# Performance work log

Hardware: AMD Instinct MI355X
Metric: run time of the kernel (lower is better)

The kernel has to match this reference:

```python
import jax, jax.numpy as jnp
import numpy as np

NUM_FEATURES = 1_000_000
EMB_DIM = 16
NUM_FIELDS = 39
CIN_SIZES = (200, 200, 200)
DNN_SIZES = (400, 400)


def setup_inputs() -> dict:
    key = jax.random.key(0)
    ks = jax.random.split(key, 16)
    B = 2048
    inp = {}
    inp["feature_ids"] = jax.random.randint(ks[0], (B, NUM_FIELDS), 0, NUM_FEATURES)
    inp["feature_vals"] = jax.random.uniform(ks[1], (B, NUM_FIELDS), dtype=jnp.float32)
    # embeddings (xavier-normal-ish scale)
    inp["emb"] = jax.random.normal(ks[2], (NUM_FEATURES, EMB_DIM), jnp.float32) * 0.02
    inp["bias_emb"] = jax.random.normal(ks[3], (NUM_FEATURES, 1), jnp.float32) * 0.02
    # CIN conv1d (kernel size 1) weights: (out, in)
    field_nums = [NUM_FIELDS]
    for i, size in enumerate(CIN_SIZES):
        cin_in = field_nums[-1] * NUM_FIELDS
        inp[f"cin_W{i}"] = jax.random.normal(ks[4 + i], (size, cin_in), jnp.float32) / np.sqrt(cin_in)
        inp[f"cin_b{i}"] = jnp.zeros((size,), jnp.float32)
        field_nums.append(size // 2 if i != len(CIN_SIZES) - 1 else size)
    # DNN linears: (out, in)
    last = NUM_FIELDS * EMB_DIM
    for i, size in enumerate(DNN_SIZES):
        inp[f"dnn_W{i}"] = jax.random.normal(ks[8 + i], (size, last), jnp.float32) / np.sqrt(last)
        inp[f"dnn_b{i}"] = jnp.zeros((size,), jnp.float32)
        last = size
    hidden_size = sum(CIN_SIZES[:-1]) // 2 + CIN_SIZES[-1]  # 400
    fc_in = hidden_size + DNN_SIZES[-1]
    inp["fc_W"] = jax.random.normal(ks[12], (1, fc_in), jnp.float32) / np.sqrt(fc_in)
    inp["fc_b"] = jnp.zeros((1,), jnp.float32)
    return inp


def _forward(feature_ids, feature_vals, emb, bias_emb,
             cin_W0, cin_b0, cin_W1, cin_b1, cin_W2, cin_b2,
             dnn_W0, dnn_b0, dnn_W1, dnn_b1, fc_W, fc_b):
    B = feature_ids.shape[0]
    inputs = emb[feature_ids] * feature_vals[:, :, None]        # [B, F, D]
    input_biases = bias_emb[feature_ids][..., 0] * feature_vals  # [B, F]

    # CIN
    Ws = (cin_W0, cin_W1, cin_W2)
    bs = (cin_b0, cin_b1, cin_b2)
    h = inputs
    finals = []
    n_layers = len(CIN_SIZES)
    for i in range(n_layers):
        size = CIN_SIZES[i]
        x = jnp.einsum('bhd,bmd->bhmd', h, inputs)              # [B, H, F, D]
        x = x.reshape(B, -1, EMB_DIM)                           # [B, H*F, D]
        x = jnp.einsum('bcd,oc->bod', x, Ws[i]) + bs[i][None, :, None]  # 1x1 conv
        x = jax.nn.relu(x)
        if i != n_layers - 1:
            h, direct = x[:, : size // 2], x[:, size // 2:]
        else:
            direct = x
        finals.append(direct)
    cin_result = jnp.sum(jnp.concatenate(finals, axis=1), axis=-1)  # [B, hidden]

    # DNN
    d = inputs.reshape(B, -1)
    d = jax.nn.relu(d @ dnn_W0.T + dnn_b0)
    d = jax.nn.relu(d @ dnn_W1.T + dnn_b1)

    out = (jnp.concatenate((cin_result, d), axis=1) @ fc_W.T + fc_b)[:, 0]
    return out + jnp.sum(input_biases, axis=1)                  # [B]


def reference(feature_ids, feature_vals, emb, bias_emb,
              cin_W0, cin_b0, cin_W1, cin_b1, cin_W2, cin_b2,
              dnn_W0, dnn_b0, dnn_W1, dnn_b1, fc_W, fc_b):
    return _forward(feature_ids, feature_vals, emb, bias_emb,
                    cin_W0, cin_b0, cin_W1, cin_b1, cin_W2, cin_b2,
                    dnn_W0, dnn_b0, dnn_W1, dnn_b1, fc_W, fc_b)
```

## Files before the change

kernel.cpp:

```cpp
#include <hip/hip_runtime.h>

#define B 2048
#define NF 39
#define D 16

typedef __bf16 bf16x8 __attribute__((ext_vector_type(8)));
typedef float f32x4 __attribute__((ext_vector_type(4)));

__device__ __forceinline__ void lds_barrier() {
  asm volatile("s_waitcnt lgkmcnt(0)" ::: "memory");
  __builtin_amdgcn_s_barrier();
}

__global__ __launch_bounds__(256) void gather_kernel(
    const int* __restrict__ fid, const float* __restrict__ fval,
    const float* __restrict__ emb, const float* __restrict__ bias_emb,
    float* __restrict__ inputs, float* __restrict__ biassum) {
  int b = blockIdx.x;
  __shared__ int ids[NF];
  __shared__ float vals[NF];
  int t = threadIdx.x;
  if (t < NF) { ids[t] = fid[b * NF + t]; vals[t] = fval[b * NF + t]; }
  __syncthreads();
  for (int i = t; i < NF * D; i += 256) {
    int f = i >> 4, d = i & 15;
    inputs[b * NF * D + i] = emb[(long)ids[f] * D + d] * vals[f];
  }
  if (t < 64) {
    float pb = (t < NF) ? bias_emb[ids[t]] * vals[t] : 0.f;
#pragma unroll
    for (int m = 32; m >= 1; m >>= 1) pb += __shfl_xor(pb, m);
    if (t == 0) biassum[b] = pb;
  }
}

__device__ __forceinline__ void prep_cin_one(const float* __restrict__ W,
                                             __bf16* __restrict__ Wg,
                                             int Hreal, int idx) {
  int l = idx & 63;
  int mt = (idx >> 6) % 13;
  int c = idx / (13 * 64);
  int o = mt * 16 + (l & 15);
  int kb = c * 32 + ((l >> 4) << 3);
  int rowlen = Hreal * 39;
  bf16x8 v;
#pragma unroll
  for (int j = 0; j < 8; ++j) {
    int k = kb + j;
    int h = k / 40;
    int m = k - h * 40;
    float val = 0.f;
    if (o < 200 && h < Hreal && m < 39) val = W[(long)o * rowlen + h * 39 + m];
    v[j] = (__bf16)val;
  }
  *reinterpret_cast<bf16x8*>(Wg + (long)idx * 8) = v;
}

__device__ __forceinline__ void prep_dnn_one(const float* __restrict__ W,
                                             __bf16* __restrict__ Wd,
                                             int IN, int idx) {
  int l = idx & 63;
  int tt = (idx >> 6) % 25;
  int c = idx / (25 * 64);
  int o = tt * 16 + (l & 15);
  int kb = c * 32 + ((l >> 4) << 3);
  bf16x8 v;
#pragma unroll
  for (int j = 0; j < 8; ++j) {
    int k = kb + j;
    v[j] = (k < IN) ? (__bf16)W[(long)o * IN + k] : (__bf16)0.f;
  }
  *reinterpret_cast<bf16x8*>(Wd + (long)idx * 8) = v;
}

#define PREP_T0 (50 * 13 * 64)
#define PREP_T12 (126 * 13 * 64)
#define PREP_T3 (20 * 25 * 64)
#define PREP_T4 (13 * 25 * 64)
#define PREP_TOTAL (PREP_T0 + 2 * PREP_T12 + PREP_T3 + PREP_T4)

__global__ void prep_all(const float* __restrict__ cW0, const float* __restrict__ cW1,
                         const float* __restrict__ cW2, const float* __restrict__ dW0,
                         const float* __restrict__ dW1, __bf16* __restrict__ Wg0,
                         __bf16* __restrict__ Wg1, __bf16* __restrict__ Wg2,
                         __bf16* __restrict__ Wd0, __bf16* __restrict__ Wd1) {
  int idx = blockIdx.x * 256 + threadIdx.x;
  if (idx < PREP_T0) { prep_cin_one(cW0, Wg0, 39, idx); return; }
  idx -= PREP_T0;
  if (idx < PREP_T12) { prep_cin_one(cW1, Wg1, 100, idx); return; }
  idx -= PREP_T12;
  if (idx < PREP_T12) { prep_cin_one(cW2, Wg2, 100, idx); return; }
  idx -= PREP_T12;
  if (idx < PREP_T3) { prep_dnn_one(dW0, Wd0, 624, idx); return; }
  idx -= PREP_T3;
  if (idx < PREP_T4) prep_dnn_one(dW1, Wd1, 400, idx);
}

__device__ __forceinline__ void form_x(const float* Hs, const float* Zs,
                                       __bf16* xbuf, int k0, int col) {
  int h = (int)((unsigned)k0 / 40u);
  int m0 = k0 - h * 40;
  float hv = Hs[h * 64 + col];
  const float4* zp = reinterpret_cast<const float4*>(Zs + col * 44 + m0);
  float4 za = zp[0], zb = zp[1];
  bf16x8 xv;
  xv[0] = (__bf16)(hv * za.x); xv[1] = (__bf16)(hv * za.y);
  xv[2] = (__bf16)(hv * za.z); xv[3] = (__bf16)(hv * za.w);
  xv[4] = (__bf16)(hv * zb.x); xv[5] = (__bf16)(hv * zb.y);
  xv[6] = (__bf16)(hv * zb.z); xv[7] = (__bf16)(hv * zb.w);
  int g = (k0 >> 3) & 7;
  *reinterpret_cast<bf16x8*>(
      reinterpret_cast<char*>(xbuf) + col * 128 + ((g * 16) ^ ((col & 7) << 4))) = xv;
}

template <int NW, int NST, int SPLIT>
__device__ __forceinline__ void cin_layer(
    float* Hs, const float* Zs, __bf16* Xs,
    const __bf16* __restrict__ Wg, const float* __restrict__ bias,
    float* __restrict__ cin_out, int col_offset, int bbase, int t) {
  constexpr int TLO = (13 * NW) >> 2;
  const int l = t & 63;
  const int q = l >> 4, dd = l & 15;

  f32x4 acc[13] = {};
  bf16x8 wf[8], wfn[8];
  const __bf16* wp = Wg + l * 8 + TLO * 512;
#pragma unroll
  for (int i = 0; i < 4; ++i)
#pragma unroll
    for (int hf = 0; hf < 2; ++hf)
      wf[i * 2 + hf] = *reinterpret_cast<const bf16x8*>(wp + hf * 6656 + i * 512);

  form_x(Hs, Zs, Xs, NW * 8, l);
  form_x(Hs, Zs, Xs, (NW + 4) * 8, l);
  lds_barrier();

  for (int s = 0; s < NST; ++s) {
    __bf16* xcur = Xs + (s & 1) * 4096;
    __bf16* xnxt = Xs + ((s + 1) & 1) * 4096;
    const bool more = (s + 1 < NST);
    if (more) {
      const __bf16* wq = wp + 13312;
#pragma unroll
      for (int i = 0; i < 4; ++i)
#pragma unroll
        for (int hf = 0; hf < 2; ++hf)
          wfn[i * 2 + hf] =
              *reinterpret_cast<const bf16x8*>(wq + hf * 6656 + i * 512);
    }
    bf16x8 bfr[4][2];
#pragma unroll
    for (int f = 0; f < 4; ++f)
#pragma unroll
      for (int hf = 0; hf < 2; ++hf) {
        int col = f * 16 + dd;
        int g = q + hf * 4;
        bfr[f][hf] = *reinterpret_cast<const bf16x8*>(
            reinterpret_cast<const char*>(xcur) + col * 128 +
            ((g * 16) ^ ((col & 7) << 4)));
      }
    if (more) {
      form_x(Hs, Zs, xnxt, (s + 1) * 64 + NW * 8, l);
      form_x(Hs, Zs, xnxt, (s + 1) * 64 + (NW + 4) * 8, l);
    }
    __builtin_amdgcn_s_setprio(1);
#pragma unroll
    for (int i = 0; i < 13; ++i) {
      const int p = 13 * NW + i;
      const int ti = (p >> 2) - TLO;
      const int f = p & 3;
      acc[i] = __builtin_amdgcn_mfma_f32_16x16x32_bf16(wf[ti * 2 + 0], bfr[f][0],
                                                       acc[i], 0, 0, 0);
      acc[i] = __builtin_amdgcn_mfma_f32_16x16x32_bf16(wf[ti * 2 + 1], bfr[f][1],
                                                       acc[i], 0, 0, 0);
    }
    __builtin_amdgcn_s_setprio(0);
    lds_barrier();
    if (more) {
#pragma unroll
      for (int i = 0; i < 8; ++i) wf[i] = wfn[i];
      wp += 13312;
    }
  }

#pragma unroll
  for (int i = 0; i < 13; ++i) {
    const int p = 13 * NW + i;
    const int tt = p >> 2, f = p & 3;
    const int b = bbase + f;
#pragma unroll
    for (int r = 0; r < 4; ++r) {
      int o = tt * 16 + q * 4 + r;
      if (o < 200) {
        float x = fmaxf(acc[i][r] + bias[o], 0.f);
        if (SPLIT && o < 100) {
          Hs[o * 64 + f * 16 + dd] = x;
        } else {
          x += __shfl_xor(x, 1);
          x += __shfl_xor(x, 2);
          x += __shfl_xor(x, 4);
          x += __shfl_xor(x, 8);
          if (dd == 0) cin_out[b * 400 + col_offset + o - (SPLIT ? 100 : 0)] = x;
        }
      }
    }
  }
  lds_barrier();
}

template <int NW>
__device__ __forceinline__ void cin_all(
    float* Hs, const float* Zs, __bf16* Xs, const __bf16* Wg0,
    const __bf16* Wg1, const __bf16* Wg2, const float* cb0, const float* cb1,
    const float* cb2, float* cinres, int bbase, int t) {
  cin_layer<NW, 25, 1>(Hs, Zs, Xs, Wg0, cb0, cinres, 0, bbase, t);
  cin_layer<NW, 63, 1>(Hs, Zs, Xs, Wg1, cb1, cinres, 100, bbase, t);
  cin_layer<NW, 63, 0>(Hs, Zs, Xs, Wg2, cb2, cinres, 200, bbase, t);
}

__global__ __launch_bounds__(256, 2) void cin_fused(
    const float* __restrict__ Zin, const __bf16* __restrict__ Wg0,
    const __bf16* __restrict__ Wg1, const __bf16* __restrict__ Wg2,
    const float* __restrict__ cb0, const float* __restrict__ cb1,
    const float* __restrict__ cb2, float* __restrict__ cinres) {
  __shared__ float Hs[101 * 64];
  __shared__ float Zs[64 * 44];
  __shared__ __bf16 Xs[2 * 64 * 64];
  const int t = threadIdx.x;
  const int bbase = blockIdx.x * 4;

  for (int i = t; i < 64 * 40; i += 256) {
    int col = i / 40, m = i - (i / 40) * 40;
    int b = bbase + (col >> 4), d = col & 15;
    Zs[col * 44 + m] = (m < NF) ? Zin[((long)b * NF + m) * 16 + d] : 0.f;
  }
  for (int i = t; i < 41 * 64; i += 256) {
    int h = i >> 6, col = i & 63;
    int b = bbase + (col >> 4), d = col & 15;
    Hs[i] = (h < NF) ? Zin[((long)b * NF + h) * 16 + d] : 0.f;
  }
  if (t < 64) Hs[100 * 64 + t] = 0.f;
  __syncthreads();

  const int w = t >> 6;
  if (w == 0) cin_all<0>(Hs, Zs, Xs, Wg0, Wg1, Wg2, cb0, cb1, cb2, cinres, bbase, t);
  else if (w == 1) cin_all<1>(Hs, Zs, Xs, Wg0, Wg1, Wg2, cb0, cb1, cb2, cinres, bbase, t);
  else if (w == 2) cin_all<2>(Hs, Zs, Xs, Wg0, Wg1, Wg2, cb0, cb1, cb2, cinres, bbase, t);
  else cin_all<3>(Hs, Zs, Xs, Wg0, Wg1, Wg2, cb0, cb1, cb2, cinres, bbase, t);
}

template <int IN>
__device__ __forceinline__ void dnn_stage_load(const float* __restrict__ x,
                                               int bg, int c, int t,
                                               float4& a, float4& b2) {
  int b = t >> 2, kb = t & 3;
  int k0 = c * 32 + kb * 8;
  if (k0 < IN) {
    const float4* p =
        reinterpret_cast<const float4*>(x + (long)(bg * 64 + b) * IN + k0);
    a = p[0];
    b2 = p[1];
  } else {
    a = make_float4(0.f, 0.f, 0.f, 0.f);
    b2 = make_float4(0.f, 0.f, 0.f, 0.f);
  }
}

__device__ __forceinline__ void dnn_stage_write(__bf16* Xs, int t, float4 a,
                                                float4 b2) {
  int b = t >> 2, kb = t & 3;
  bf16x8 v;
  v[0] = (__bf16)a.x;  v[1] = (__bf16)a.y;  v[2] = (__bf16)a.z;  v[3] = (__bf16)a.w;
  v[4] = (__bf16)b2.x; v[5] = (__bf16)b2.y; v[6] = (__bf16)b2.z; v[7] = (__bf16)b2.w;
  *reinterpret_cast<bf16x8*>(Xs + ((kb * 64 + b) << 3)) = v;
}

template <int IN, int NCH>
__global__ __launch_bounds__(256) void dnn_mfma2(
    const float* __restrict__ x, const __bf16* __restrict__ Wd,
    const float* __restrict__ bias, float* __restrict__ out) {
  __shared__ __bf16 Xs[2 * 2048];
  const int bg = blockIdx.x / 25;
  const int tile = blockIdx.x - bg * 25;
  const int t = threadIdx.x;
  const int w = t >> 6, l = t & 63;
  const int q = l >> 4, dd = l & 15;
  const __bf16* wl = Wd + l * 8;

  f32x4 acc = {};
  bf16x8 wf = *reinterpret_cast<const bf16x8*>(wl + (long)(tile * 64) * 8);

  float4 ra, rb;
  dnn_stage_load<IN>(x, bg, 0, t, ra, rb);
  dnn_stage_write(Xs, t, ra, rb);
  lds_barrier();

  for (int c = 0; c < NCH; ++c) {
    __bf16* cur = Xs + (c & 1) * 2048;
    __bf16* nxt = Xs + ((c + 1) & 1) * 2048;
    const bool more = (c + 1 < NCH);
    bf16x8 wfn;
    if (more) {
      dnn_stage_load<IN>(x, bg, c + 1, t, ra, rb);
      wfn = *reinterpret_cast<const bf16x8*>(
          wl + (long)(((c + 1) * 25 + tile) * 64) * 8);
    }
    bf16x8 bfr = *reinterpret_cast<const bf16x8*>(cur + ((q * 64 + w * 16 + dd) << 3));
    acc = __builtin_amdgcn_mfma_f32_16x16x32_bf16(wf, bfr, acc, 0, 0, 0);
    if (more) dnn_stage_write(nxt, t, ra, rb);
    lds_barrier();
    if (more) wf = wfn;
  }

  const int b = bg * 64 + w * 16 + dd;
#pragma unroll
  for (int r = 0; r < 4; ++r) {
    int o = tile * 16 + q * 4 + r;
    out[(long)b * 400 + o] = fmaxf(acc[r] + bias[o], 0.f);
  }
}

__global__ __launch_bounds__(256) void final_kernel(
    const float* __restrict__ cin, const float* __restrict__ d1,
    const float* __restrict__ fcW, const float* __restrict__ fcb,
    const float* __restrict__ biassum, float* __restrict__ out) {
  int b = blockIdx.x, t = threadIdx.x;
  float p = 0.f;
  for (int i = t; i < 800; i += 256) {
    float v = (i < 400) ? cin[b * 400 + i] : d1[b * 400 + (i - 400)];
    p += v * fcW[i];
  }
#pragma unroll
  for (int m = 32; m >= 1; m >>= 1) p += __shfl_xor(p, m);
  __shared__ float red[4];
  if ((t & 63) == 0) red[t >> 6] = p;
  __syncthreads();
  if (t == 0) out[b] = red[0] + red[1] + red[2] + red[3] + fcb[0] + biassum[b];
}

extern "C" void kernel_launch(void* const* d_in, const int* in_sizes, int n_in,
                              void* d_out, int out_size, void* d_ws,
                              size_t ws_size, hipStream_t stream) {
  (void)in_sizes; (void)n_in; (void)out_size; (void)ws_size;
  const int* fid = (const int*)d_in[0];
  const float* fval = (const float*)d_in[1];
  const float* emb = (const float*)d_in[2];
  const float* bias_emb = (const float*)d_in[3];
  const float* cW0 = (const float*)d_in[4];
  const float* cb0 = (const float*)d_in[5];
  const float* cW1 = (const float*)d_in[6];
  const float* cb1 = (const float*)d_in[7];
  const float* cW2 = (const float*)d_in[8];
  const float* cb2 = (const float*)d_in[9];
  const float* dW0 = (const float*)d_in[10];
  const float* db0 = (const float*)d_in[11];
  const float* dW1 = (const float*)d_in[12];
  const float* db1 = (const float*)d_in[13];
  const float* fcW = (const float*)d_in[14];
  const float* fcb = (const float*)d_in[15];
  float* out = (float*)d_out;

  float* ws = (float*)d_ws;
  float* inputs = ws;  ws += B * NF * D;
  float* biassum = ws; ws += B;
  float* cinres = ws;  ws += B * 400;
  float* dd0 = ws;     ws += B * 400;
  float* dd1 = ws;     ws += B * 400;
  __bf16* Wg0 = (__bf16*)ws; ws += (50 * 13 * 64 * 8) / 2;
  __bf16* Wg1 = (__bf16*)ws; ws += (126 * 13 * 64 * 8) / 2;
  __bf16* Wg2 = (__bf16*)ws; ws += (126 * 13 * 64 * 8) / 2;
  __bf16* Wd0 = (__bf16*)ws; ws += (20 * 25 * 64 * 8) / 2;
  __bf16* Wd1 = (__bf16*)ws; ws += (13 * 25 * 64 * 8) / 2;

  gather_kernel<<<B, 256, 0, stream>>>(fid, fval, emb, bias_emb, inputs, biassum);

  prep_all<<<(PREP_TOTAL + 255) / 256, 256, 0, stream>>>(
      cW0, cW1, cW2, dW0, dW1, Wg0, Wg1, Wg2, Wd0, Wd1);

  cin_fused<<<B / 4, 256, 0, stream>>>(inputs, Wg0, Wg1, Wg2, cb0, cb1, cb2, cinres);

  dnn_mfma2<624, 20><<<32 * 25, 256, 0, stream>>>(inputs, Wd0, db0, dd0);
  dnn_mfma2<400, 13><<<32 * 25, 256, 0, stream>>>(dd0, Wd1, db1, dd1);

  final_kernel<<<B, 256, 0, stream>>>(cinres, dd1, fcW, fcb, biassum, out);
}
```

Before: 198.5 us.

## Merge CIN kernel and first DNN layer into one heterogeneous launch

Fuses the CIN kernel and the first DNN linear layer into a single launch. Block indices below 512 run the CIN path and the remaining 800 blocks run the DNN layer-0 GEMM, sharing one dynamically partitioned shared-memory buffer. The goal is to overlap the two independent stages on the GPU and remove one launch boundary and its tail. In exchange, the DNN blocks now carry the larger CIN shared-memory footprint and its launch bounds, which may reduce their occupancy.

New measurement: 199.6 us. About the same (+0.5%).

```diff
diff --git a/kernel.cpp b/kernel.cpp
--- a/kernel.cpp
+++ b/kernel.cpp
@@ -218,37 +218,6 @@
   cin_layer<NW, 63, 0>(Hs, Zs, Xs, Wg2, cb2, cinres, 200, bbase, t);
 }
 
-__global__ __launch_bounds__(256, 2) void cin_fused(
-    const float* __restrict__ Zin, const __bf16* __restrict__ Wg0,
-    const __bf16* __restrict__ Wg1, const __bf16* __restrict__ Wg2,
-    const float* __restrict__ cb0, const float* __restrict__ cb1,
-    const float* __restrict__ cb2, float* __restrict__ cinres) {
-  __shared__ float Hs[101 * 64];
-  __shared__ float Zs[64 * 44];
-  __shared__ __bf16 Xs[2 * 64 * 64];
-  const int t = threadIdx.x;
-  const int bbase = blockIdx.x * 4;
-
-  for (int i = t; i < 64 * 40; i += 256) {
-    int col = i / 40, m = i - (i / 40) * 40;
-    int b = bbase + (col >> 4), d = col & 15;
-    Zs[col * 44 + m] = (m < NF) ? Zin[((long)b * NF + m) * 16 + d] : 0.f;
-  }
-  for (int i = t; i < 41 * 64; i += 256) {
-    int h = i >> 6, col = i & 63;
-    int b = bbase + (col >> 4), d = col & 15;
-    Hs[i] = (h < NF) ? Zin[((long)b * NF + h) * 16 + d] : 0.f;
-  }
-  if (t < 64) Hs[100 * 64 + t] = 0.f;
-  __syncthreads();
-
-  const int w = t >> 6;
-  if (w == 0) cin_all<0>(Hs, Zs, Xs, Wg0, Wg1, Wg2, cb0, cb1, cb2, cinres, bbase, t);
-  else if (w == 1) cin_all<1>(Hs, Zs, Xs, Wg0, Wg1, Wg2, cb0, cb1, cb2, cinres, bbase, t);
-  else if (w == 2) cin_all<2>(Hs, Zs, Xs, Wg0, Wg1, Wg2, cb0, cb1, cb2, cinres, bbase, t);
-  else cin_all<3>(Hs, Zs, Xs, Wg0, Wg1, Wg2, cb0, cb1, cb2, cinres, bbase, t);
-}
-
 template <int IN>
 __device__ __forceinline__ void dnn_stage_load(const float* __restrict__ x,
                                                int bg, int c, int t,
@@ -276,13 +245,10 @@
 }
 
 template <int IN, int NCH>
-__global__ __launch_bounds__(256) void dnn_mfma2(
+__device__ __forceinline__ void dnn_body(
     const float* __restrict__ x, const __bf16* __restrict__ Wd,
-    const float* __restrict__ bias, float* __restrict__ out) {
-  __shared__ __bf16 Xs[2 * 2048];
-  const int bg = blockIdx.x / 25;
-  const int tile = blockIdx.x - bg * 25;
-  const int t = threadIdx.x;
+    const float* __restrict__ bias, float* __restrict__ out, __bf16* Xs,
+    int bg, int tile, int t) {
   const int w = t >> 6, l = t & 63;
   const int q = l >> 4, dd = l & 15;
   const __bf16* wl = Wd + l * 8;
@@ -318,6 +284,56 @@
     int o = tile * 16 + q * 4 + r;
     out[(long)b * 400 + o] = fmaxf(acc[r] + bias[o], 0.f);
   }
+}
+
+__global__ __launch_bounds__(256, 2) void cin_dnn0(
+    const float* __restrict__ Zin, const __bf16* __restrict__ Wg0,
+    const __bf16* __restrict__ Wg1, const __bf16* __restrict__ Wg2,
+    const float* __restrict__ cb0, const float* __restrict__ cb1,
+    const float* __restrict__ cb2, float* __restrict__ cinres,
+    const __bf16* __restrict__ Wd0, const float* __restrict__ db0,
+    float* __restrict__ dd0) {
+  __shared__ alignas(16) char smem[53760];
+  const int t = threadIdx.x;
+
+  if (blockIdx.x >= 512) {
+    int blk = blockIdx.x - 512;
+    dnn_body<624, 20>(Zin, Wd0, db0, dd0, (__bf16*)smem, blk / 25, blk % 25, t);
+    return;
+  }
+
+  float* Hs = (float*)smem;
+  float* Zs = (float*)(smem + 25856);
+  __bf16* Xs = (__bf16*)(smem + 37120);
+  const int bbase = blockIdx.x * 4;
+
+  for (int i = t; i < 64 * 40; i += 256) {
+    int col = i / 40, m = i - (i / 40) * 40;
+    int b = bbase + (col >> 4), d = col & 15;
+    Zs[col * 44 + m] = (m < NF) ? Zin[((long)b * NF + m) * 16 + d] : 0.f;
+  }
+  for (int i = t; i < 41 * 64; i += 256) {
+    int h = i >> 6, col = i & 63;
+    int b = bbase + (col >> 4), d = col & 15;
+    Hs[i] = (h < NF) ? Zin[((long)b * NF + h) * 16 + d] : 0.f;
+  }
+  if (t < 64) Hs[100 * 64 + t] = 0.f;
+  __syncthreads();
+
+  const int w = t >> 6;
+  if (w == 0) cin_all<0>(Hs, Zs, Xs, Wg0, Wg1, Wg2, cb0, cb1, cb2, cinres, bbase, t);
+  else if (w == 1) cin_all<1>(Hs, Zs, Xs, Wg0, Wg1, Wg2, cb0, cb1, cb2, cinres, bbase, t);
+  else if (w == 2) cin_all<2>(Hs, Zs, Xs, Wg0, Wg1, Wg2, cb0, cb1, cb2, cinres, bbase, t);
+  else cin_all<3>(Hs, Zs, Xs, Wg0, Wg1, Wg2, cb0, cb1, cb2, cinres, bbase, t);
+}
+
+template <int IN, int NCH>
+__global__ __launch_bounds__(256) void dnn_mfma2(
+    const float* __restrict__ x, const __bf16* __restrict__ Wd,
+    const float* __restrict__ bias, float* __restrict__ out) {
+  __shared__ __bf16 Xs[2 * 2048];
+  dnn_body<IN, NCH>(x, Wd, bias, out, Xs, blockIdx.x / 25, blockIdx.x % 25,
+                    threadIdx.x);
 }
 
 __global__ __launch_bounds__(256) void final_kernel(
@@ -377,10 +393,10 @@
   prep_all<<<(PREP_TOTAL + 255) / 256, 256, 0, stream>>>(
       cW0, cW1, cW2, dW0, dW1, Wg0, Wg1, Wg2, Wd0, Wd1);
 
-  cin_fused<<<B / 4, 256, 0, stream>>>(inputs, Wg0, Wg1, Wg2, cb0, cb1, cb2, cinres);
-
-  dnn_mfma2<624, 20><<<32 * 25, 256, 0, stream>>>(inputs, Wd0, db0, dd0);
-  dnn_mfma2<400, 13><<<32 * 25, 256, 0, stream>>>(dd0, Wd1, db1, dd1);
+  cin_dnn0<<<512 + 800, 256, 0, stream>>>(inputs, Wg0, Wg1, Wg2, cb0, cb1, cb2,
+                                          cinres, Wd0, db0, dd0);
+
+  dnn_mfma2<400, 13><<<800, 256, 0, stream>>>(dd0, Wd1, db1, dd1);
 
   final_kernel<<<B, 256, 0, stream>>>(cinres, dd1, fcW, fcb, biassum, out);
 }
```
